# Kernel optimization log

Measured on AMD Instinct MI355X. Metric: run time of the kernel, lower is better.

The kernel has to match this reference:

```python
import jax, jax.numpy as jnp
import numpy as np
import math

B, S, D = 2, 2048, 2048
H, HK = 32, 8          # query heads, kv heads
HD = D // H            # 64
REP = H // HK          # 4


def setup_inputs() -> dict:
    key = jax.random.key(0)
    ks = jax.random.split(key, 6)
    x = jax.random.normal(ks[0], (B, S, D), jnp.float32)
    # RoPE tables, rotate_half convention: halves duplicated along last dim
    inv_freq = 1.0 / (10000.0 ** (jnp.arange(0, HD, 2, dtype=jnp.float32) / HD))
    freqs = jnp.arange(S, dtype=jnp.float32)[:, None] * inv_freq[None, :]  # [S, HD/2]
    cos = jnp.concatenate([jnp.cos(freqs), jnp.cos(freqs)], axis=-1)       # [S, HD]
    sin = jnp.concatenate([jnp.sin(freqs), jnp.sin(freqs)], axis=-1)
    attn_mask = jnp.tril(jnp.ones((S, S), dtype=bool))
    std = 1.0 / math.sqrt(D)
    wq = jax.random.normal(ks[1], (D, D), jnp.float32) * std
    wk = jax.random.normal(ks[2], (HK * HD, D), jnp.float32) * std
    wv = jax.random.normal(ks[3], (HK * HD, D), jnp.float32) * std
    wo = jax.random.normal(ks[4], (D, D), jnp.float32) * std
    return {"x": x, "cos": cos, "sin": sin, "attn_mask": attn_mask,
            "wq": wq, "wk": wk, "wv": wv, "wo": wo}


def _rotate_half(t):
    h = t.shape[-1] // 2
    return jnp.concatenate([-t[..., h:], t[..., :h]], axis=-1)


def reference(x, cos, sin, attn_mask, wq, wk, wv, wo):
    b, s, d = x.shape
    q = (x @ wq.T).reshape(b, s, H, HD).transpose(0, 2, 1, 3)    # [b,H,s,hd]
    k = (x @ wk.T).reshape(b, s, HK, HD).transpose(0, 2, 1, 3)   # [b,HK,s,hd]
    v = (x @ wv.T).reshape(b, s, HK, HD).transpose(0, 2, 1, 3)
    c = cos[:s][None, None]
    sn = sin[:s][None, None]
    q = q * c + _rotate_half(q) * sn
    k = k * c + _rotate_half(k) * sn
    # GQA: group query heads instead of repeat_interleave'ing KV
    # repeat_interleave order == reshape (HK, REP): heads [g*REP : (g+1)*REP] share kv group g
    qg = q.reshape(b, HK, REP, s, HD)
    scores = jnp.einsum('bgrsd,bgtd->bgrst', qg, k) / math.sqrt(HD)  # [b,HK,REP,s,s]
    m = attn_mask[None, None, None, :, :]
    scores = jnp.where(m, scores, -jnp.inf)
    attn = jax.nn.softmax(scores, axis=-1)
    out = jnp.einsum('bgrst,bgtd->bgrsd', attn, v)                  # [b,HK,REP,s,hd]
    out = out.reshape(b, H, s, HD).transpose(0, 2, 1, 3).reshape(b, s, d)
    return out @ wo.T
```

## Files before the change

kernel.cpp:

```cpp
#include <hip/hip_runtime.h>
#include <hip/hip_bf16.h>
#include <math.h>

typedef __hip_bfloat16 bf16;
typedef __attribute__((ext_vector_type(8))) short bf16x8;
typedef __attribute__((ext_vector_type(4))) short short4v;
typedef __attribute__((ext_vector_type(4))) float f32x4;
typedef __attribute__((ext_vector_type(4))) unsigned int u32x4;

static constexpr int B = 2, S = 2048, D = 2048, H = 32, HK = 8, HD = 64;
static constexpr int M = B * S;
static constexpr int NKV = HK * HD;
static constexpr int QKV3 = D + 2 * NKV;
static constexpr float SCALE2 = 0.125f * 1.44269504f;

__device__ __forceinline__ short bfbits(float x) {
  bf16 h = __float2bfloat16(x);
  return *reinterpret_cast<short*>(&h);
}

__device__ __forceinline__ float bf2f(short bits) {
  unsigned int u = ((unsigned int)(unsigned short)bits) << 16;
  return __builtin_bit_cast(float, u);
}

__device__ __forceinline__ void gl_lds16(const bf16* gp, bf16* lp) {
  __builtin_amdgcn_global_load_lds(
      (const __attribute__((address_space(1))) unsigned int*)(const void*)gp,
      (__attribute__((address_space(3))) unsigned int*)(void*)lp, 16, 0, 0);
}

struct alignas(8) bf4 { bf16 v[4]; };
static constexpr int N4_X  = M * D / 4;
static constexpr int N4_WQ = D * D / 4;
static constexpr int N4_WK = NKV * D / 4;
static constexpr int E0 = N4_X;
static constexpr int E1 = E0 + N4_WQ;
static constexpr int E2 = E1 + N4_WK;
static constexpr int E3 = E2 + N4_WK;
static constexpr int E4 = E3 + N4_WQ;
__global__ __launch_bounds__(256) void cast_all_kernel(const float* __restrict__ x,
                                                       const float* __restrict__ wq,
                                                       const float* __restrict__ wk,
                                                       const float* __restrict__ wv,
                                                       const float* __restrict__ wo,
                                                       bf16* __restrict__ xb,
                                                       bf16* __restrict__ wqkv,
                                                       bf16* __restrict__ wob) {
  int i = blockIdx.x * 256 + threadIdx.x;
  int stride = gridDim.x * 256;
  for (; i < E4; i += stride) {
    const float* s; bf16* d; int j;
    if (i < E0)      { s = x;  d = xb;   j = i; }
    else if (i < E1) { s = wq; d = wqkv; j = i - E0; }
    else if (i < E2) { s = wk; d = wqkv + (size_t)N4_WQ * 4; j = i - E1; }
    else if (i < E3) { s = wv; d = wqkv + (size_t)(N4_WQ + N4_WK) * 4; j = i - E2; }
    else             { s = wo; d = wob;  j = i - E3; }
    float4 f = reinterpret_cast<const float4*>(s)[j];
    bf4 o;
    o.v[0] = __float2bfloat16(f.x);
    o.v[1] = __float2bfloat16(f.y);
    o.v[2] = __float2bfloat16(f.z);
    o.v[3] = __float2bfloat16(f.w);
    reinterpret_cast<bf4*>(d)[j] = o;
  }
}

template <bool OUT_F32>
__global__ __launch_bounds__(256) void gemm_bt_kernel(const bf16* __restrict__ A,
                                                      const bf16* __restrict__ Bt,
                                                      void* __restrict__ C,
                                                      int Ndim, int Kdim) {
  __shared__ __align__(16) bf16 As[128][64];
  __shared__ __align__(16) bf16 Bs[128][64];
  const int tid = threadIdx.x;
  const int lane = tid & 63;
  const int w = tid >> 6;
  const int wm = w >> 1, wn = w & 1;
  const int r16 = lane & 15, g = lane >> 4;
  const int bm = blockIdx.y, bn = blockIdx.x;
  f32x4 acc[4][4] = {};

  const int nk = Kdim >> 6;
  for (int kt = 0; kt < nk; ++kt) {
    __syncthreads();
#pragma unroll
    for (int i = 0; i < 4; ++i) {
      int u = tid + i * 256;
      int rr = u >> 3, c8 = u & 7;
      int c8s = c8 ^ (rr & 7);
      gl_lds16(&A[(size_t)(bm * 128 + rr) * Kdim + kt * 64 + c8s * 8], &As[0][0] + (size_t)u * 8);
      gl_lds16(&Bt[(size_t)(bn * 128 + rr) * Kdim + kt * 64 + c8s * 8], &Bs[0][0] + (size_t)u * 8);
    }
    __syncthreads();
#pragma unroll
    for (int kc = 0; kc < 2; ++kc) {
      bf16x8 af[4], bfr[4];
      const int kq = kc * 4 + g;
#pragma unroll
      for (int m = 0; m < 4; ++m) {
        int ra = wm * 64 + m * 16 + r16;
        af[m] = *reinterpret_cast<const bf16x8*>(&As[ra][(kq ^ (ra & 7)) * 8]);
        int rb = wn * 64 + m * 16 + r16;
        bfr[m] = *reinterpret_cast<const bf16x8*>(&Bs[rb][(kq ^ (rb & 7)) * 8]);
      }
#pragma unroll
      for (int m = 0; m < 4; ++m)
#pragma unroll
        for (int n = 0; n < 4; ++n)
          acc[m][n] = __builtin_amdgcn_mfma_f32_16x16x32_bf16(af[m], bfr[n], acc[m][n], 0, 0, 0);
    }
  }
  const int row0 = bm * 128 + wm * 64 + g * 4;
  const int col0 = bn * 128 + wn * 64 + r16;
#pragma unroll
  for (int m = 0; m < 4; ++m)
#pragma unroll
    for (int n = 0; n < 4; ++n)
#pragma unroll
      for (int j = 0; j < 4; ++j) {
        size_t idx = (size_t)(row0 + m * 16 + j) * Ndim + col0 + n * 16;
        if (OUT_F32)
          reinterpret_cast<float*>(C)[idx] = acc[m][n][j];
        else
          reinterpret_cast<bf16*>(C)[idx] = __float2bfloat16(acc[m][n][j]);
      }
}

__global__ __launch_bounds__(256) void rope_k_kernel(bf16* __restrict__ t,
                                                     const float* __restrict__ cosb,
                                                     const float* __restrict__ sinb) {
  int idx = blockIdx.x * 256 + threadIdx.x;
  int i = idx & 31;
  int rest = idx >> 5;
  int hh = rest & 7;
  int s = (rest >> 3) % S;
  int b = rest / (8 * S);
  size_t base = ((size_t)b * S + s) * QKV3 + D + hh * HD;
  float x0 = __bfloat162float(t[base + i]);
  float x1 = __bfloat162float(t[base + i + 32]);
  float c = cosb[s * HD + i];
  float sn = sinb[s * HD + i];
  t[base + i] = __float2bfloat16(x0 * c - x1 * sn);
  t[base + i + 32] = __float2bfloat16(x1 * c + x0 * sn);
}

__global__ __launch_bounds__(256) void transpose_v_kernel(const bf16* __restrict__ qkv,
                                                          bf16* __restrict__ vt) {
  __shared__ bf16 tile[64][65];
  const int st = blockIdx.x;
  const int bk = blockIdx.y;
  const int b = bk >> 3, hk = bk & 7;
  const int tid = threadIdx.x;
#pragma unroll
  for (int i = 0; i < 16; ++i) {
    int idx = tid + i * 256;
    int rs = idx >> 6, c = idx & 63;
    tile[rs][c] = qkv[((size_t)b * S + st * 64 + rs) * QKV3 + (D + NKV) + hk * HD + c];
  }
  __syncthreads();
#pragma unroll
  for (int i = 0; i < 16; ++i) {
    int idx = tid + i * 256;
    int rh = idx >> 6, cs = idx & 63;
    int blk = cs >> 5, kvl = cs & 31;
    int pos = ((kvl >> 2) & 3) * 8 + ((kvl >> 4) << 2) + (kvl & 3);
    vt[(((size_t)b * HK + hk) * HD + rh) * S + st * 64 + blk * 32 + pos] = tile[cs][rh];
  }
}

__global__ __launch_bounds__(256, 2) void attn_kernel(const bf16* __restrict__ qkv,
                                                      const bf16* __restrict__ vt,
                                                      const float* __restrict__ cosb,
                                                      const float* __restrict__ sinb,
                                                      bf16* __restrict__ ao) {
  __shared__ __align__(16) bf16 Ksh[2][64 * 64];
  __shared__ __align__(16) bf16 Vsh[2][64 * 64];
  const int u = blockIdx.x;
  const int y = blockIdx.y;
  const int b = y >> 3, hk = y & 7;
  const int tid = threadIdx.x;
  const int w = tid >> 6;
  const int h = hk * 4 + w;
  const int lane = tid & 63;
  const int r = lane & 15, g = lane >> 4;

  const bf16* qp  = qkv + ((size_t)b * S) * QKV3 + h * HD;
  const bf16* kvp = qkv + ((size_t)b * S) * QKV3 + D + hk * HD;
  const bf16* vtp = vt + (((size_t)b * HK + hk) * HD) * S;
  const int srow = tid >> 3;
  const int sc8 = tid & 7;

  bf16x8 ones;
#pragma unroll
  for (int j = 0; j < 8; ++j) ones[j] = (short)0x3F80;

  auto stage64 = [&](int buf, int kv0) {
#pragma unroll
    for (int i = 0; i < 2; ++i) {
      int rr = srow + i * 32;
      int cs = sc8 ^ (rr & 7);
      gl_lds16(&kvp[(size_t)(kv0 + rr) * QKV3 + cs * 8], &Ksh[buf][((size_t)rr * 8 + sc8) * 8]);
    }
#pragma unroll
    for (int i = 0; i < 2; ++i) {
      int rr = srow + i * 32;
      int cs = sc8 ^ (rr & 7);
      gl_lds16(&vtp[(size_t)rr * S + kv0 + cs * 8], &Vsh[buf][((size_t)rr * 8 + sc8) * 8]);
    }
  };

  for (int pass = 0; pass < 2; ++pass) {
    const int qb = pass ? (2016 - u * 32) : (u * 32);
    bf16x8 qfr[2][2];
#pragma unroll
    for (int qq = 0; qq < 2; ++qq) {
      const int srowq = qb + qq * 16 + r;
      bf16x8 f0 = *reinterpret_cast<const bf16x8*>(&qp[(size_t)srowq * QKV3 + g * 8]);
      bf16x8 f1 = *reinterpret_cast<const bf16x8*>(&qp[(size_t)srowq * QKV3 + 32 + g * 8]);
      float4 c0 = reinterpret_cast<const float4*>(&cosb[(size_t)srowq * HD + g * 8])[0];
      float4 c1 = reinterpret_cast<const float4*>(&cosb[(size_t)srowq * HD + g * 8])[1];
      float4 s0 = reinterpret_cast<const float4*>(&sinb[(size_t)srowq * HD + g * 8])[0];
      float4 s1 = reinterpret_cast<const float4*>(&sinb[(size_t)srowq * HD + g * 8])[1];
      float cc[8] = {c0.x, c0.y, c0.z, c0.w, c1.x, c1.y, c1.z, c1.w};
      float ss[8] = {s0.x, s0.y, s0.z, s0.w, s1.x, s1.y, s1.z, s1.w};
#pragma unroll
      for (int j = 0; j < 8; ++j) {
        float x0 = bf2f(f0[j]), x1 = bf2f(f1[j]);
        qfr[qq][0][j] = bfbits((x0 * cc[j] - x1 * ss[j]) * SCALE2);
        qfr[qq][1][j] = bfbits((x1 * cc[j] + x0 * ss[j]) * SCALE2);
      }
    }

    f32x4 o[4][2] = {};
    f32x4 ol[2] = {};
    const int kv_end = qb + 32;
    const int nch = (kv_end + 63) >> 6;

    auto chunk = [&](int CUR, int cc, bool lastc) {
      const int kv0 = cc * 64;
      if (!lastc) stage64(CUR ^ 1, kv0 + 64);
      f32x4 scv[4][2] = {};
      __builtin_amdgcn_s_setprio(1);
#pragma unroll
      for (int f = 0; f < 4; ++f) {
        const int row = f * 16 + r;
#pragma unroll
        for (int hc = 0; hc < 2; ++hc) {
          bf16x8 kf = *reinterpret_cast<const bf16x8*>(
              &Ksh[CUR][(size_t)row * 64 + (((hc * 4 + g) ^ (r & 7)) * 8)]);
          scv[f][0] = __builtin_amdgcn_mfma_f32_16x16x32_bf16(kf, qfr[0][hc], scv[f][0], 0, 0, 0);
          scv[f][1] = __builtin_amdgcn_mfma_f32_16x16x32_bf16(kf, qfr[1][hc], scv[f][1], 0, 0, 0);
        }
      }
      __builtin_amdgcn_s_setprio(0);
      if (lastc) {
#pragma unroll
        for (int qq = 0; qq < 2; ++qq) {
          const int lim = qb + qq * 16 + r - kv0;
#pragma unroll
          for (int f = 0; f < 4; ++f)
#pragma unroll
            for (int j = 0; j < 4; ++j)
              if (f * 16 + g * 4 + j > lim) scv[f][qq][j] = -1e30f;
        }
      }
#pragma unroll
      for (int blk = 0; blk < 2; ++blk) {
        u32x4 pk0, pk1;
#pragma unroll
        for (int pj = 0; pj < 4; ++pj) {
          const int f = blk * 2 + (pj >> 1);
          const int j0 = (pj & 1) * 2;
          float a0 = __builtin_amdgcn_exp2f(scv[f][0][j0]);
          float a1 = __builtin_amdgcn_exp2f(scv[f][0][j0 + 1]);
          pk0[pj] = (__builtin_bit_cast(unsigned int, a0) >> 16) |
                    (__builtin_bit_cast(unsigned int, a1) & 0xffff0000u);
          float b0 = __builtin_amdgcn_exp2f(scv[f][1][j0]);
          float b1 = __builtin_amdgcn_exp2f(scv[f][1][j0 + 1]);
          pk1[pj] = (__builtin_bit_cast(unsigned int, b0) >> 16) |
                    (__builtin_bit_cast(unsigned int, b1) & 0xffff0000u);
        }
        bf16x8 pb0 = __builtin_bit_cast(bf16x8, pk0);
        bf16x8 pb1 = __builtin_bit_cast(bf16x8, pk1);
        __builtin_amdgcn_s_setprio(1);
        ol[0] = __builtin_amdgcn_mfma_f32_16x16x32_bf16(ones, pb0, ol[0], 0, 0, 0);
        ol[1] = __builtin_amdgcn_mfma_f32_16x16x32_bf16(ones, pb1, ol[1], 0, 0, 0);
#pragma unroll
        for (int d = 0; d < 4; ++d) {
          bf16x8 vf = *reinterpret_cast<const bf16x8*>(
              &Vsh[CUR][(size_t)(d * 16 + r) * 64 + (((blk * 4 + g) ^ (r & 7)) * 8)]);
          o[d][0] = __builtin_amdgcn_mfma_f32_16x16x32_bf16(vf, pb0, o[d][0], 0, 0, 0);
          o[d][1] = __builtin_amdgcn_mfma_f32_16x16x32_bf16(vf, pb1, o[d][1], 0, 0, 0);
        }
        __builtin_amdgcn_s_setprio(0);
      }
      __syncthreads();
    };

    stage64(0, 0);
    __syncthreads();
    int c = 0;
    for (; c + 2 <= nch; c += 2) {
      chunk(0, c, c == nch - 1);
      chunk(1, c + 1, c + 1 == nch - 1);
    }
    if (c < nch) chunk(0, c, true);

#pragma unroll
    for (int qq = 0; qq < 2; ++qq) {
      float inv = 1.0f / ol[qq][0];
#pragma unroll
      for (int d = 0; d < 4; ++d) {
        short4v ov;
        ov[0] = bfbits(o[d][qq][0] * inv);
        ov[1] = bfbits(o[d][qq][1] * inv);
        ov[2] = bfbits(o[d][qq][2] * inv);
        ov[3] = bfbits(o[d][qq][3] * inv);
        *reinterpret_cast<short4v*>(
            &ao[(((size_t)b * S + qb + qq * 16 + r) * H + h) * HD + d * 16 + g * 4]) = ov;
      }
    }
  }
}

extern "C" void kernel_launch(void* const* d_in, const int* in_sizes, int n_in,
                              void* d_out, int out_size, void* d_ws, size_t ws_size,
                              hipStream_t stream) {
  (void)in_sizes; (void)n_in; (void)out_size; (void)ws_size;
  const float* x    = (const float*)d_in[0];
  const float* cosb = (const float*)d_in[1];
  const float* sinb = (const float*)d_in[2];
  const float* wq   = (const float*)d_in[4];
  const float* wk   = (const float*)d_in[5];
  const float* wv   = (const float*)d_in[6];
  const float* wo   = (const float*)d_in[7];

  char* ws = (char*)d_ws;
  size_t off = 0;
  auto alloc = [&](size_t elems) {
    bf16* p = (bf16*)(ws + off);
    off = (off + elems * sizeof(bf16) + 255) & ~(size_t)255;
    return p;
  };
  bf16* xb    = alloc((size_t)M * D);
  bf16* wqkvb = alloc((size_t)QKV3 * D);
  bf16* wob   = alloc((size_t)D * D);
  bf16* qkvb  = alloc((size_t)M * QKV3);
  bf16* vtb   = alloc((size_t)B * HK * HD * S);
  bf16* aob   = alloc((size_t)M * D);

  cast_all_kernel<<<dim3(2048), dim3(256), 0, stream>>>(x, wq, wk, wv, wo, xb, wqkvb, wob);

  gemm_bt_kernel<false><<<dim3(QKV3 / 128, M / 128), 256, 0, stream>>>(xb, wqkvb, qkvb, QKV3, D);

  rope_k_kernel<<<dim3(B * S * 8 * 32 / 256), 256, 0, stream>>>(qkvb, cosb, sinb);

  transpose_v_kernel<<<dim3(S / 64, B * HK), 256, 0, stream>>>(qkvb, vtb);

  attn_kernel<<<dim3(32, B * HK), 256, 0, stream>>>(qkvb, vtb, cosb, sinb, aob);

  gemm_bt_kernel<true><<<dim3(D / 128, M / 128), 256, 0, stream>>>(aob, wob, d_out, D, D);
}
```

Baseline: 175.5 us.

## Add 256x256 double-buffered GEMM with XOR-swizzled LDS for QKV projection

Replaces the 128x128 tile GEMM for the fused QKV projection with a new 512-thread kernel using 256x256 tiles and double-buffered LDS loaded directly from global memory. Shared-memory chunks are XOR-swizzled to avoid bank conflicts, and block indices are remapped for L2 locality. Explicit waitcnt and barrier scheduling overlaps loads with MFMA work. The grid drops to 16x12=192 blocks at one block per CU, so fewer blocks than CUs may leave some units idle.

```diff
diff --git a/kernel.cpp b/kernel.cpp
--- a/kernel.cpp
+++ b/kernel.cpp
@@ -66,6 +66,98 @@
   }
 }
 
+__global__ __launch_bounds__(512, 1) void gemm256_kernel(const bf16* __restrict__ A,
+                                                         const bf16* __restrict__ Bt,
+                                                         bf16* __restrict__ C,
+                                                         int Ndim, int Kdim) {
+  __shared__ __align__(16) bf16 As[2][256 * 64];
+  __shared__ __align__(16) bf16 Bs[2][256 * 64];
+  const int tid = threadIdx.x;
+  const int wv = tid >> 6;
+  const int wm = wv >> 2, wn = wv & 3;
+  const int lane = tid & 63;
+  const int r16 = lane & 15, g = lane >> 4;
+
+  const int nwg = gridDim.x;
+  const int lin = blockIdx.x;
+  const int swz = (lin & 7) * (nwg >> 3) + (lin >> 3);
+  const int gx = Ndim >> 8;
+  const int bn = swz % gx;
+  const int bm = swz / gx;
+
+  f32x4 acc[8][4] = {};
+  const int nk = Kdim >> 6;
+
+  auto stage = [&](int buf, int t) {
+#pragma unroll
+    for (int i = 0; i < 4; ++i) {
+      int u = tid + i * 512;
+      int rr = u >> 3, c8 = u & 7;
+      int c8s = c8 ^ (rr & 7);
+      gl_lds16(&A[(size_t)(bm * 256 + rr) * Kdim + t * 64 + c8s * 8], &As[buf][0] + (size_t)u * 8);
+    }
+#pragma unroll
+    for (int i = 0; i < 4; ++i) {
+      int u = tid + i * 512;
+      int rr = u >> 3, c8 = u & 7;
+      int c8s = c8 ^ (rr & 7);
+      gl_lds16(&Bt[(size_t)(bn * 256 + rr) * Kdim + t * 64 + c8s * 8], &Bs[buf][0] + (size_t)u * 8);
+    }
+  };
+
+  auto gtile = [&](int CUR, int t) {
+    if (t + 1 < nk) asm volatile("s_waitcnt vmcnt(8)" ::: "memory");
+    else            asm volatile("s_waitcnt vmcnt(0)" ::: "memory");
+    __builtin_amdgcn_sched_barrier(0);
+    __builtin_amdgcn_s_barrier();
+    __builtin_amdgcn_sched_barrier(0);
+    __builtin_amdgcn_s_setprio(1);
+#pragma unroll
+    for (int kc = 0; kc < 2; ++kc) {
+      bf16x8 af[8], bfr[4];
+      const int kq = kc * 4 + g;
+#pragma unroll
+      for (int m = 0; m < 8; ++m) {
+        int ra = wm * 128 + m * 16 + r16;
+        af[m] = *reinterpret_cast<const bf16x8*>(&As[CUR][(size_t)ra * 64 + ((kq ^ (ra & 7)) * 8)]);
+      }
+#pragma unroll
+      for (int n = 0; n < 4; ++n) {
+        int rb = wn * 64 + n * 16 + r16;
+        bfr[n] = *reinterpret_cast<const bf16x8*>(&Bs[CUR][(size_t)rb * 64 + ((kq ^ (rb & 7)) * 8)]);
+      }
+#pragma unroll
+      for (int m = 0; m < 8; ++m)
+#pragma unroll
+        for (int n = 0; n < 4; ++n)
+          acc[m][n] = __builtin_amdgcn_mfma_f32_16x16x32_bf16(af[m], bfr[n], acc[m][n], 0, 0, 0);
+    }
+    __builtin_amdgcn_s_setprio(0);
+    asm volatile("s_waitcnt lgkmcnt(0)" ::: "memory");
+    __builtin_amdgcn_sched_barrier(0);
+    __builtin_amdgcn_s_barrier();
+    __builtin_amdgcn_sched_barrier(0);
+    if (t + 2 < nk) stage(CUR, t + 2);
+  };
+
+  stage(0, 0);
+  stage(1, 1);
+  for (int t = 0; t < nk; t += 2) {
+    gtile(0, t);
+    gtile(1, t + 1);
+  }
+
+  const int row0 = bm * 256 + wm * 128 + g * 4;
+  const int col0 = bn * 256 + wn * 64 + r16;
+#pragma unroll
+  for (int m = 0; m < 8; ++m)
+#pragma unroll
+    for (int n = 0; n < 4; ++n)
+#pragma unroll
+      for (int j = 0; j < 4; ++j)
+        C[(size_t)(row0 + m * 16 + j) * Ndim + col0 + n * 16] = __float2bfloat16(acc[m][n][j]);
+}
+
 template <bool OUT_F32>
 __global__ __launch_bounds__(256) void gemm_bt_kernel(const bf16* __restrict__ A,
                                                       const bf16* __restrict__ Bt,
@@ -352,7 +444,7 @@
 
   cast_all_kernel<<<dim3(2048), dim3(256), 0, stream>>>(x, wq, wk, wv, wo, xb, wqkvb, wob);
 
-  gemm_bt_kernel<false><<<dim3(QKV3 / 128, M / 128), 256, 0, stream>>>(xb, wqkvb, qkvb, QKV3, D);
+  gemm256_kernel<<<dim3((M / 256) * (QKV3 / 256)), dim3(512), 0, stream>>>(xb, wqkvb, qkvb, QKV3, D);
 
   rope_k_kernel<<<dim3(B * S * 8 * 32 / 256), 256, 0, stream>>>(qkvb, cosb, sinb);
 
```

Result: slower. 184.9 us (+5.3%).

## Fuse K RoPE and V transpose into QKV projection GEMM epilogue

Applied to the files above, without the earlier changes.

Adds a dedicated QKV GEMM whose epilogue applies RoPE to K columns in registers and writes V directly in the permuted transposed layout used by attention. This removes two separate kernels and their extra global-memory round trips and launches. It risks uncoalesced short stores for the V transpose and branch divergence across column ranges in the epilogue.

```diff
diff --git a/kernel.cpp b/kernel.cpp
--- a/kernel.cpp
+++ b/kernel.cpp
@@ -66,6 +66,107 @@
   }
 }
 
+__global__ __launch_bounds__(256) void gemm_qkv_kernel(const bf16* __restrict__ A,
+                                                       const bf16* __restrict__ Wt,
+                                                       bf16* __restrict__ qkv,
+                                                       bf16* __restrict__ vt,
+                                                       const float* __restrict__ cosb,
+                                                       const float* __restrict__ sinb) {
+  __shared__ __align__(16) bf16 As[128][64];
+  __shared__ __align__(16) bf16 Bs[128][64];
+  const int tid = threadIdx.x;
+  const int lane = tid & 63;
+  const int w = tid >> 6;
+  const int wm = w >> 1, wn = w & 1;
+  const int r16 = lane & 15, g = lane >> 4;
+  const int bm = blockIdx.y, bn = blockIdx.x;
+  f32x4 acc[4][4] = {};
+
+  const int nk = D >> 6;
+  for (int kt = 0; kt < nk; ++kt) {
+    __syncthreads();
+#pragma unroll
+    for (int i = 0; i < 4; ++i) {
+      int u = tid + i * 256;
+      int rr = u >> 3, c8 = u & 7;
+      int c8s = c8 ^ (rr & 7);
+      gl_lds16(&A[(size_t)(bm * 128 + rr) * D + kt * 64 + c8s * 8], &As[0][0] + (size_t)u * 8);
+      gl_lds16(&Wt[(size_t)(bn * 128 + rr) * D + kt * 64 + c8s * 8], &Bs[0][0] + (size_t)u * 8);
+    }
+    __syncthreads();
+#pragma unroll
+    for (int kc = 0; kc < 2; ++kc) {
+      bf16x8 af[4], bfr[4];
+      const int kq = kc * 4 + g;
+#pragma unroll
+      for (int m = 0; m < 4; ++m) {
+        int ra = wm * 64 + m * 16 + r16;
+        af[m] = *reinterpret_cast<const bf16x8*>(&As[ra][(kq ^ (ra & 7)) * 8]);
+        int rb = wn * 64 + m * 16 + r16;
+        bfr[m] = *reinterpret_cast<const bf16x8*>(&Bs[rb][(kq ^ (rb & 7)) * 8]);
+      }
+#pragma unroll
+      for (int m = 0; m < 4; ++m)
+#pragma unroll
+        for (int n = 0; n < 4; ++n)
+          acc[m][n] = __builtin_amdgcn_mfma_f32_16x16x32_bf16(af[m], bfr[n], acc[m][n], 0, 0, 0);
+    }
+  }
+
+  const int row0 = bm * 128 + wm * 64 + g * 4;
+  const int col0 = bn * 128 + wn * 64 + r16;
+  if (col0 < D) {
+#pragma unroll
+    for (int m = 0; m < 4; ++m)
+#pragma unroll
+      for (int n = 0; n < 4; ++n)
+#pragma unroll
+        for (int j = 0; j < 4; ++j)
+          qkv[(size_t)(row0 + m * 16 + j) * QKV3 + col0 + n * 16] =
+              __float2bfloat16(acc[m][n][j]);
+  } else if (col0 < D + NKV) {
+#pragma unroll
+    for (int m = 0; m < 4; ++m)
+#pragma unroll
+      for (int j = 0; j < 4; ++j) {
+        const int tok = row0 + m * 16 + j;
+        const int s = tok & (S - 1);
+        const float c0 = cosb[(size_t)s * HD + r16];
+        const float c1 = cosb[(size_t)s * HD + 16 + r16];
+        const float s0 = sinb[(size_t)s * HD + r16];
+        const float s1 = sinb[(size_t)s * HD + 16 + r16];
+        const float x0a = acc[m][0][j], x1a = acc[m][2][j];
+        const float x0b = acc[m][1][j], x1b = acc[m][3][j];
+        bf16* rp = &qkv[(size_t)tok * QKV3 + col0];
+        rp[0]  = __float2bfloat16(x0a * c0 - x1a * s0);
+        rp[16] = __float2bfloat16(x0b * c1 - x1b * s1);
+        rp[32] = __float2bfloat16(x1a * c0 + x0a * s0);
+        rp[48] = __float2bfloat16(x1b * c1 + x0b * s1);
+      }
+  } else {
+#pragma unroll
+    for (int m = 0; m < 4; ++m) {
+      const int tok = row0 + m * 16;
+      const int b = tok >> 11;
+      const int sg = tok & (S - 1);
+      const int blk = sg >> 5, kvl0 = sg & 31;
+      const int pos0 = ((kvl0 >> 2) & 3) * 8 + ((kvl0 >> 4) << 2);
+#pragma unroll
+      for (int n = 0; n < 4; ++n) {
+        const int vch = col0 + n * 16 - (D + NKV);
+        const int hk = vch >> 6, hd = vch & 63;
+        short4v ov;
+        ov[0] = bfbits(acc[m][n][0]);
+        ov[1] = bfbits(acc[m][n][1]);
+        ov[2] = bfbits(acc[m][n][2]);
+        ov[3] = bfbits(acc[m][n][3]);
+        *reinterpret_cast<short4v*>(
+            &vt[(((size_t)b * HK + hk) * HD + hd) * S + blk * 32 + pos0]) = ov;
+      }
+    }
+  }
+}
+
 template <bool OUT_F32>
 __global__ __launch_bounds__(256) void gemm_bt_kernel(const bf16* __restrict__ A,
                                                       const bf16* __restrict__ Bt,
@@ -125,48 +226,6 @@
         else
           reinterpret_cast<bf16*>(C)[idx] = __float2bfloat16(acc[m][n][j]);
       }
-}
-
-__global__ __launch_bounds__(256) void rope_k_kernel(bf16* __restrict__ t,
-                                                     const float* __restrict__ cosb,
-                                                     const float* __restrict__ sinb) {
-  int idx = blockIdx.x * 256 + threadIdx.x;
-  int i = idx & 31;
-  int rest = idx >> 5;
-  int hh = rest & 7;
-  int s = (rest >> 3) % S;
-  int b = rest / (8 * S);
-  size_t base = ((size_t)b * S + s) * QKV3 + D + hh * HD;
-  float x0 = __bfloat162float(t[base + i]);
-  float x1 = __bfloat162float(t[base + i + 32]);
-  float c = cosb[s * HD + i];
-  float sn = sinb[s * HD + i];
-  t[base + i] = __float2bfloat16(x0 * c - x1 * sn);
-  t[base + i + 32] = __float2bfloat16(x1 * c + x0 * sn);
-}
-
-__global__ __launch_bounds__(256) void transpose_v_kernel(const bf16* __restrict__ qkv,
-                                                          bf16* __restrict__ vt) {
-  __shared__ bf16 tile[64][65];
-  const int st = blockIdx.x;
-  const int bk = blockIdx.y;
-  const int b = bk >> 3, hk = bk & 7;
-  const int tid = threadIdx.x;
-#pragma unroll
-  for (int i = 0; i < 16; ++i) {
-    int idx = tid + i * 256;
-    int rs = idx >> 6, c = idx & 63;
-    tile[rs][c] = qkv[((size_t)b * S + st * 64 + rs) * QKV3 + (D + NKV) + hk * HD + c];
-  }
-  __syncthreads();
-#pragma unroll
-  for (int i = 0; i < 16; ++i) {
-    int idx = tid + i * 256;
-    int rh = idx >> 6, cs = idx & 63;
-    int blk = cs >> 5, kvl = cs & 31;
-    int pos = ((kvl >> 2) & 3) * 8 + ((kvl >> 4) << 2) + (kvl & 3);
-    vt[(((size_t)b * HK + hk) * HD + rh) * S + st * 64 + blk * 32 + pos] = tile[cs][rh];
-  }
 }
 
 __global__ __launch_bounds__(256, 2) void attn_kernel(const bf16* __restrict__ qkv,
@@ -352,11 +411,8 @@
 
   cast_all_kernel<<<dim3(2048), dim3(256), 0, stream>>>(x, wq, wk, wv, wo, xb, wqkvb, wob);
 
-  gemm_bt_kernel<false><<<dim3(QKV3 / 128, M / 128), 256, 0, stream>>>(xb, wqkvb, qkvb, QKV3, D);
-
-  rope_k_kernel<<<dim3(B * S * 8 * 32 / 256), 256, 0, stream>>>(qkvb, cosb, sinb);
-
-  transpose_v_kernel<<<dim3(S / 64, B * HK), 256, 0, stream>>>(qkvb, vtb);
+  gemm_qkv_kernel<<<dim3(QKV3 / 128, M / 128), 256, 0, stream>>>(xb, wqkvb, qkvb, vtb,
+                                                                 cosb, sinb);
 
   attn_kernel<<<dim3(32, B * HK), 256, 0, stream>>>(qkvb, vtb, cosb, sinb, aob);
 
```

Result: slower. 187.7 us (+7.0%).
